# Optimization experiments

Measured on AMD Instinct MI355X. Metric: run time of the kernel, lower is better.

## Reference

```python
import math
import jax, jax.numpy as jnp
import numpy as np

HOP = 256
N_FFT = 1024
SR = 24000
B = 8
T = 1200          # feature frames
L = T * HOP       # 307200 audio samples
K_REV = 8192
BINS = N_FFT // 2 + 1


def setup_inputs() -> dict:
    key = jax.random.key(0)
    k1, k2, k3, k4, k5 = jax.random.split(key, 5)
    # realistic voiced f0 in [50, 400] Hz (forward gates on f0 > 20 Hz)
    f0 = 50.0 + 350.0 * jax.random.uniform(k1, (B, T), dtype=jnp.float32)
    env_per = jax.random.uniform(k2, (B, BINS, T), dtype=jnp.float32)
    env_noi = 0.1 * jax.random.uniform(k3, (B, BINS, T), dtype=jnp.float32)
    rev = 0.01 * jax.random.normal(k4, (B, K_REV), dtype=jnp.float32)
    # stands in for torch.rand_like(imp) inside forward (uniform [0,1))
    noi = jax.random.uniform(k5, (B, L), dtype=jnp.float32)
    # periodic Hann window, as torch.hann_window(n_fft)
    window = (0.5 - 0.5 * jnp.cos(2.0 * jnp.pi * jnp.arange(N_FFT) / N_FFT)).astype(jnp.float32)
    return {"f0": f0, "env_per": env_per, "env_noi": env_noi, "rev": rev, "noi": noi, "window": window}


def _interp_linear(x, scale):
    # torch F.interpolate(mode='linear', align_corners=False)
    Lx = x.shape[-1]
    out_len = Lx * scale
    src = (jnp.arange(out_len, dtype=jnp.float32) + 0.5) / scale - 0.5
    src = jnp.clip(src, 0.0, Lx - 1)
    i0 = jnp.floor(src).astype(jnp.int32)
    i1 = jnp.minimum(i0 + 1, Lx - 1)
    w = src - i0.astype(jnp.float32)
    return x[:, i0] * (1.0 - w) + x[:, i1] * w


def _stft(x, window):
    # torch.stft(center=True, pad_mode='reflect', return_complex=True)
    pad = N_FFT // 2
    xp = jnp.pad(x, ((0, 0), (pad, pad)), mode='reflect')
    n_frames = 1 + (xp.shape[-1] - N_FFT) // HOP
    idx = jnp.arange(n_frames)[:, None] * HOP + jnp.arange(N_FFT)[None, :]
    frames = xp[:, idx] * window                      # [B, F, N_FFT]
    return jnp.fft.rfft(frames, axis=-1).transpose(0, 2, 1)  # [B, BINS, F]


def _istft(spec, window):
    # torch.istft(center=True): windowed overlap-add with window-square normalization
    frames = jnp.fft.irfft(spec.transpose(0, 2, 1), n=N_FFT, axis=-1) * window  # [B, F, N_FFT]
    Bc, Fr, _ = frames.shape
    out_len = N_FFT + HOP * (Fr - 1)
    idx = (jnp.arange(Fr)[:, None] * HOP + jnp.arange(N_FFT)[None, :]).reshape(-1)
    out = jnp.zeros((Bc, out_len), frames.dtype).at[:, idx].add(frames.reshape(Bc, -1))
    wsq = jnp.zeros((out_len,), frames.dtype).at[idx].add(jnp.tile(window ** 2, Fr))
    out = out / jnp.where(wsq > 1e-11, wsq, 1.0)
    pad = N_FFT // 2
    return out[:, pad:out_len - pad]


def _min_phase(amp, eps=1e-5):
    # homomorphic minimum-phase reconstruction from real amplitude envelope
    # amp: [B, BINS, F]  ->  complex spectrum exp(rfft(lifted real cepstrum))
    log_amp = jnp.log(jnp.maximum(amp, eps))
    cep = jnp.fft.irfft(log_amp, n=N_FFT, axis=1)     # [B, N_FFT, F] real cepstrum
    lift = jnp.concatenate([
        jnp.ones((1,), jnp.float32),
        2.0 * jnp.ones((N_FFT // 2 - 1,), jnp.float32),
        jnp.ones((1,), jnp.float32),
        jnp.zeros((N_FFT // 2 - 1,), jnp.float32),
    ])
    return jnp.exp(jnp.fft.rfft(cep * lift[None, :, None], axis=1))  # [B, BINS, F]


def _fft_convolve(signal, kernel):
    # DDSP-style FFT convolution: zero-pad signal right, kernel left, multiply spectra
    Ls = signal.shape[-1]
    sig = jnp.pad(signal, ((0, 0), (0, Ls)))
    ker = jnp.pad(kernel, ((0, 0), (2 * Ls - kernel.shape[-1], 0)))
    out = jnp.fft.irfft(jnp.fft.rfft(sig) * jnp.fft.rfft(ker), n=2 * Ls)
    return out[:, Ls:]


def reference(f0, env_per, env_noi, rev, noi, window):
    env_per = jnp.pad(env_per, ((0, 0), (0, 0), (1, 0)))   # [B, BINS, T+1]
    env_noi = jnp.pad(env_noi, ((0, 0), (0, 0), (1, 0)))
    # sample-rate f0 track and impulse amplitude scale
    f0_up = _interp_linear(f0, HOP)                        # [B, L]
    imp_scale = jax.lax.rsqrt(jnp.maximum(f0_up, 20.0)) * math.sqrt(SR)
    # impulse train: fire where the running phase wraps past an integer
    phase = jnp.cumsum(f0_up, axis=-1) / SR
    saw = jnp.mod(phase, 1.0)
    imp = (saw - jnp.roll(saw, 1, axis=-1) < 0.0).astype(jnp.float32)
    imp = imp.at[:, 0].set(0.0)
    imp = imp * imp_scale
    imp_stft = _stft(imp, window)                          # [B, BINS, T+1]
    noi_stft = _stft(noi, window)
    # voiced/unvoiced gating of the periodic envelope
    mask = (jnp.pad(f0, ((0, 0), (1, 0)))[:, None, :] > 20.0).astype(jnp.float32)
    env_per = env_per * mask
    voi_stft = imp_stft * _min_phase(env_per) + noi_stft * env_noi
    voi = _istft(voi_stft, window)                         # [B, L]
    voi = _fft_convolve(voi, rev)                          # [B, L]
    return voi
```

## Files before the change

### kernel.cpp

```cpp
#include <hip/hip_runtime.h>
#include <math.h>

#define BB 8
#define TT 1200
#define NFFT 1024
#define BINS 513
#define LTOT 307200
#define KREV 8192
#define NFRM 34
#define NSAMP 8960
#define OUTOFF 299008
#define SQRT_SR 154.91933384829668f

#define OFF_FR   0
#define OFF_CW   278528
#define OFF_FW   350208
#define OFF_TW   421888

#define PHI(i) ((i) ^ ((i) >> 5))

__device__ __forceinline__ int rev4_10(int n) {
    int r = (int)(__brev((unsigned)n) >> 22);
    return ((r & 0x155) << 1) | ((r & 0x2AA) >> 1);
}

__device__ __forceinline__ void dif4(float* re, float* im,
                                     const float* twr, const float* twi,
                                     float dir, int u, bool act) {
#pragma unroll 1
    for (int s = 0; s < 5; ++s) {
        const int q = 256 >> (2 * s);
        const int sh = 8 - 2 * s;
        if (s < 2) __syncthreads();
        else       asm volatile("s_waitcnt lgkmcnt(0)" ::: "memory");
        if (act) {
            int t = u & (q - 1);
            int base = ((u >> sh) << (sh + 2)) | t;
            int i0 = PHI(base), i1 = PHI(base + q), i2 = PHI(base + 2 * q), i3 = PHI(base + 3 * q);
            float ar = re[i0], ai = im[i0];
            float br = re[i1], bi = im[i1];
            float cr = re[i2], ci = im[i2];
            float dr = re[i3], di = im[i3];
            float t0r = ar + cr, t0i = ai + ci;
            float t1r = ar - cr, t1i = ai - ci;
            float t2r = br + dr, t2i = bi + di;
            float t3r = br - dr, t3i = bi - di;
            float y0r = t0r + t2r, y0i = t0i + t2i;
            float y2r = t0r - t2r, y2i = t0i - t2i;
            float y1r = t1r - dir * t3i, y1i = t1i + dir * t3r;
            float y3r = t1r + dir * t3i, y3i = t1i - dir * t3r;
            float c1 = twr[2 * q - 1 + t], s1 = twi[2 * q - 1 + t];
            float c2 = twr[q - 1 + t],     s2 = twi[q - 1 + t];
            float w1r = c1, w1i = dir * s1;
            float w2r = c2, w2i = dir * s2;
            float w3r = c1 * c2 - s1 * s2;
            float w3i = dir * (c1 * s2 + s1 * c2);
            re[i0] = y0r;                       im[i0] = y0i;
            re[i1] = y1r * w1r - y1i * w1i;     im[i1] = y1r * w1i + y1i * w1r;
            re[i2] = y2r * w2r - y2i * w2i;     im[i2] = y2r * w2i + y2i * w2r;
            re[i3] = y3r * w3r - y3i * w3i;     im[i3] = y3r * w3i + y3i * w3r;
        }
    }
    __syncthreads();
}

__device__ __forceinline__ void dit4(float* re, float* im,
                                     const float* twr, const float* twi,
                                     float dir, int u, bool act) {
#pragma unroll 1
    for (int s = 0; s < 5; ++s) {
        const int q = 1 << (2 * s);
        const int sh = 2 * s;
        if (s == 0 || s == 4) __syncthreads();
        else                  asm volatile("s_waitcnt lgkmcnt(0)" ::: "memory");
        if (act) {
            int t = u & (q - 1);
            int base = ((u >> sh) << (sh + 2)) | t;
            int i0 = PHI(base), i1 = PHI(base + q), i2 = PHI(base + 2 * q), i3 = PHI(base + 3 * q);
            float c1 = twr[2 * q - 1 + t], s1 = twi[2 * q - 1 + t];
            float c2 = twr[q - 1 + t],     s2 = twi[q - 1 + t];
            float w1r = c1, w1i = dir * s1;
            float w2r = c2, w2i = dir * s2;
            float w3r = c1 * c2 - s1 * s2;
            float w3i = dir * (c1 * s2 + s1 * c2);
            float ar = re[i0], ai = im[i0];
            float xr = re[i1], xi = im[i1];
            float yr = re[i2], yi = im[i2];
            float zr = re[i3], zi = im[i3];
            float br = xr * w1r - xi * w1i, bi = xr * w1i + xi * w1r;
            float cr = yr * w2r - yi * w2i, ci = yr * w2i + yi * w2r;
            float dr = zr * w3r - zi * w3i, di = zr * w3i + zi * w3r;
            float t0r = ar + cr, t0i = ai + ci;
            float t1r = ar - cr, t1i = ai - ci;
            float t2r = br + dr, t2i = bi + di;
            float t3r = br - dr, t3i = bi - di;
            re[i0] = t0r + t2r;            im[i0] = t0i + t2i;
            re[i2] = t0r - t2r;            im[i2] = t0i - t2i;
            re[i1] = t1r - dir * t3i;      im[i1] = t1i + dir * t3r;
            re[i3] = t1r + dir * t3i;      im[i3] = t1i - dir * t3r;
        }
    }
    __syncthreads();
}

#define LV1 0
#define LV2 4480
#define LV3 6720
#define LV4 7840
#define LV5 8400
#define LV6 8680
#define LV7 8820
#define LV8 8890
#define LV9 8925
#define LV10 8942
#define LV11 8950
#define LV12 8954
#define LV13 8956

__global__ __launch_bounds__(1024) void k0(const float* __restrict__ f0,
                                           float* __restrict__ W) {
    const int b = blockIdx.x;
    const int tid = threadIdx.x;
    __shared__ float F[NSAMP];
    __shared__ float L[8957];

    if (b == 0 && tid < 1023) {
        int x = tid;
        int hb = 31 - __clz(x + 1);
        int half = 1 << hb;
        int t = (x + 1) - half;
        float a = 3.14159265358979323846f * ((float)t / (float)half);
        float sv, cv; sincosf(a, &sv, &cv);
        W[OFF_TW + x] = cv;
        W[OFF_TW + 1023 + x] = sv;
    }

    for (int i = tid; i < NSAMP; i += 1024) {
        float src = __fsub_rn(__fdiv_rn(__fadd_rn((float)i, 0.5f), 256.0f), 0.5f);
        src = fminf(fmaxf(src, 0.0f), (float)(TT - 1));
        int i0 = (int)floorf(src);
        int i1 = i0 + 1; if (i1 > TT - 1) i1 = TT - 1;
        float w = __fsub_rn(src, (float)i0);
        float a0 = __fmul_rn(f0[b * TT + i0], __fsub_rn(1.0f, w));
        float a1 = __fmul_rn(f0[b * TT + i1], w);
        F[i] = __fadd_rn(a0, a1);
    }
    __syncthreads();
    for (int j = tid; j < 2240; j += 1024) {
        float a = __fadd_rn(F[4*j],     F[4*j + 1]);
        float c = __fadd_rn(F[4*j + 2], F[4*j + 3]);
        L[LV1 + 2*j] = a; L[LV1 + 2*j + 1] = c;
        L[LV2 + j] = __fadd_rn(a, c);
    }
    __syncthreads();
    if (tid < 560) {
        int j = tid;
        float a = __fadd_rn(L[LV2 + 4*j],     L[LV2 + 4*j + 1]);
        float c = __fadd_rn(L[LV2 + 4*j + 2], L[LV2 + 4*j + 3]);
        L[LV3 + 2*j] = a; L[LV3 + 2*j + 1] = c;
        L[LV4 + j] = __fadd_rn(a, c);
    }
    __syncthreads();
    if (tid < 140) {
        int j = tid;
        float a = __fadd_rn(L[LV4 + 4*j],     L[LV4 + 4*j + 1]);
        float c = __fadd_rn(L[LV4 + 4*j + 2], L[LV4 + 4*j + 3]);
        L[LV5 + 2*j] = a; L[LV5 + 2*j + 1] = c;
        L[LV6 + j] = __fadd_rn(a, c);
    }
    __syncthreads();
    if (tid < 35) {
        int j = tid;
        float a = __fadd_rn(L[LV6 + 4*j],     L[LV6 + 4*j + 1]);
        float c = __fadd_rn(L[LV6 + 4*j + 2], L[LV6 + 4*j + 3]);
        L[LV7 + 2*j] = a; L[LV7 + 2*j + 1] = c;
        L[LV8 + j] = __fadd_rn(a, c);
    }
    __syncthreads();
    if (tid < 9) {
        int j = tid;
        if (j < 8) {
            float a = __fadd_rn(L[LV8 + 4*j],     L[LV8 + 4*j + 1]);
            float c = __fadd_rn(L[LV8 + 4*j + 2], L[LV8 + 4*j + 3]);
            L[LV9 + 2*j] = a; L[LV9 + 2*j + 1] = c;
            L[LV10 + j] = __fadd_rn(a, c);
        } else {
            L[LV9 + 16] = __fadd_rn(L[LV8 + 32], L[LV8 + 33]);
        }
    }
    __syncthreads();
    if (tid == 0) {
        float a0 = __fadd_rn(L[LV10 + 0], L[LV10 + 1]);
        float a1 = __fadd_rn(L[LV10 + 2], L[LV10 + 3]);
        float a2 = __fadd_rn(L[LV10 + 4], L[LV10 + 5]);
        float a3 = __fadd_rn(L[LV10 + 6], L[LV10 + 7]);
        L[LV11 + 0] = a0; L[LV11 + 1] = a1; L[LV11 + 2] = a2; L[LV11 + 3] = a3;
        float b0 = __fadd_rn(a0, a1), b1 = __fadd_rn(a2, a3);
        L[LV12 + 0] = b0; L[LV12 + 1] = b1;
        L[LV13 + 0] = __fadd_rn(b0, b1);
    }
    __syncthreads();
    {
        const int offs[14] = {0, LV1, LV2, LV3, LV4, LV5, LV6, LV7, LV8, LV9, LV10, LV11, LV12, LV13};
        for (int p = tid; p < NSAMP; p += 1024) {
            int n = p + 1;
            float acc = 0.f; int pos = 0; bool first = true;
#pragma unroll
            for (int k = 13; k >= 1; --k) {
                if ((n >> k) & 1) {
                    float t = L[offs[k] + (pos >> k)];
                    acc = first ? t : __fadd_rn(acc, t);
                    first = false;
                    pos += (1 << k);
                }
            }
            if (n & 1) {
                float t = F[pos];
                acc = first ? t : __fadd_rn(acc, t);
            }
            W[OFF_CW + b * NSAMP + p] = acc;
            W[OFF_FW + b * NSAMP + p] = F[p];
        }
    }
}

__global__ __launch_bounds__(512) void kfrm(const float* __restrict__ f0,
                                            const float* __restrict__ env_per,
                                            const float* __restrict__ env_noi,
                                            const float* __restrict__ noi,
                                            const float* __restrict__ win,
                                            float* __restrict__ W,
                                            float* __restrict__ out) {
    const int bid = blockIdx.x;
    const int tid = threadIdx.x;
    const int b = bid / 17;
    const int fp = (bid - b * 17) * 2;
    const int fg = fp + 1;

    __shared__ __align__(16) float SMEM[8208];
    __shared__ float cw[1281], fw[1281];
    __shared__ float twr[1023], twi[1023];

    const int idxF = (fp > 0) ? (fp - 1) : 0;
    const int idxG = fg - 1;
    float pfEpF = 0.f, pfEpG = 0.f, pfEpF2 = 0.f, pfEpG2 = 0.f;
    {
        pfEpF = env_per[((size_t)(b * BINS + tid)) * TT + idxF];
        pfEpG = env_per[((size_t)(b * BINS + tid)) * TT + idxG];
        if (tid == 0) {
            pfEpF2 = env_per[((size_t)(b * BINS + 512)) * TT + idxF];
            pfEpG2 = env_per[((size_t)(b * BINS + 512)) * TT + idxG];
        }
    }
    const float pfF0F = f0[b * TT + idxF];
    const float pfF0G = f0[b * TT + idxG];
    int ktmp0 = rev4_10(tid);
    const int kk0 = (ktmp0 <= 512) ? ktmp0 : 1024 - ktmp0;
    int ktmp1 = rev4_10(tid + 512);
    const int kk1 = (ktmp1 <= 512) ? ktmp1 : 1024 - ktmp1;
    const float pfEnF0 = env_noi[((size_t)(b * BINS + kk0)) * TT + idxF];
    const float pfEnG0 = env_noi[((size_t)(b * BINS + kk0)) * TT + idxG];
    const float pfEnF1 = env_noi[((size_t)(b * BINS + kk1)) * TT + idxF];
    const float pfEnG1 = env_noi[((size_t)(b * BINS + kk1)) * TT + idxG];
    int iF0 = 256 * fp + tid - 512; if (iF0 < 0) iF0 = -iF0;
    const int iF1 = 256 * fp + tid;
    int iG0 = 256 * fg + tid - 512; if (iG0 < 0) iG0 = -iG0;
    const int iG1 = 256 * fg + tid;
    const float pfNoiF0 = noi[(size_t)b * LTOT + iF0];
    const float pfNoiF1 = noi[(size_t)b * LTOT + iF1];
    const float pfNoiG0 = noi[(size_t)b * LTOT + iG0];
    const float pfNoiG1 = noi[(size_t)b * LTOT + iG1];
    const float pfWin0 = win[tid];
    const float pfWin1 = win[tid + 512];

    for (int x = tid; x < 1023; x += 512) {
        twr[x] = W[OFF_TW + x];
        twi[x] = W[OFF_TW + 1023 + x];
    }
    const int cbase = (fp >= 3) ? (256 * fp - 513) : 0;
    for (int w = tid; w < 1281; w += 512) {
        int p = cbase + w;
        if (p < NSAMP) {
            cw[w] = W[OFF_CW + b * NSAMP + p];
            fw[w] = W[OFF_FW + b * NSAMP + p];
        }
    }

    float* wr_  = SMEM;
    float* wi_  = SMEM + 1024;
    float* zfr  = SMEM + 2048;
    float* zfi  = SMEM + 3072;
    float* zgr  = SMEM + 4096;
    float* zgi  = SMEM + 5120;
    float* mpfr = SMEM + 6144;
    float* mpfi = SMEM + 6660;
    float* mpgr = SMEM + 7176;
    float* mpgi = SMEM + 7692;
    const int u = tid & 255;
    const bool lo = (tid < 256);

    {
        const bool gF = (fp > 0) && (pfF0F > 20.0f);
        const bool gG = (pfF0G > 20.0f);
        mpfr[tid] = logf(fmaxf(gF ? pfEpF : 0.0f, 1e-5f));
        mpgr[tid] = logf(fmaxf(gG ? pfEpG : 0.0f, 1e-5f));
        if (tid == 0) {
            mpfr[512] = logf(fmaxf(gF ? pfEpF2 : 0.0f, 1e-5f));
            mpgr[512] = logf(fmaxf(gG ? pfEpG2 : 0.0f, 1e-5f));
        }
    }
    __syncthreads();
#pragma unroll 1
    for (int r = 0; r < 2; ++r) {
        int n = tid + (r << 9);
        int kv = (n <= 512) ? n : 1024 - n;
        wr_[PHI(n)] = mpfr[kv];
        wi_[PHI(n)] = mpgr[kv];
    }
    dif4(wr_, wi_, twr, twi, -1.f, u, lo);
    const float inv = 1.0f / 1024.0f;
#pragma unroll 1
    for (int r = 0; r < 2; ++r) {
        int p = tid + (r << 9);
        int n = rev4_10(p);
        float wgt = (n == 0 || n == 512) ? inv : ((n < 512) ? 2.0f * inv : 0.0f);
        wr_[PHI(p)] *= wgt;
        wi_[PHI(p)] *= wgt;
    }
    dit4(wr_, wi_, twr, twi, -1.f, u, lo);
    for (int k = tid; k < BINS; k += 512) {
        int mk = (1024 - k) & 1023;
        float yr = wr_[PHI(k)], yi = wi_[PHI(k)];
        float ymr = wr_[PHI(mk)], ymi = -wi_[PHI(mk)];
        float Lfr = 0.5f * (yr + ymr), Lfi = 0.5f * (yi + ymi);
        float dr = yr - ymr, di = yi - ymi;
        float Lgr = 0.5f * di, Lgi = -0.5f * dr;
        float ef = expf(Lfr);
        mpfr[k] = ef * cosf(Lfi); mpfi[k] = ef * sinf(Lfi);
        float eg = expf(Lgr);
        mpgr[k] = eg * cosf(Lgi); mpgi[k] = eg * sinf(Lgi);
    }
    __syncthreads();
#pragma unroll 1
    for (int r = 0; r < 2; ++r) {
        const int n = tid + (r << 9);
        const float wv = r ? pfWin1 : pfWin0;
#pragma unroll 1
        for (int h = 0; h < 2; ++h) {
            int i = h ? (r ? iG1 : iG0) : (r ? iF1 : iF0);
            float nv = h ? (r ? pfNoiG1 : pfNoiG0) : (r ? pfNoiF1 : pfNoiF0);
            float v = 0.0f;
            if (i > 0) {
                int iw = i - cbase;
                float ph  = __fdiv_rn(cw[iw], 24000.0f);
                float sw  = __fsub_rn(ph, floorf(ph));
                float ph2 = __fdiv_rn(cw[iw - 1], 24000.0f);
                float sw2 = __fsub_rn(ph2, floorf(ph2));
                if (__fsub_rn(sw, sw2) < 0.0f)
                    v = __fmul_rn(__fdiv_rn(1.0f, __fsqrt_rn(fmaxf(fw[iw], 20.0f))), SQRT_SR);
            }
            float* zr = h ? zgr : zfr;
            float* zi = h ? zgi : zfi;
            zr[PHI(n)] = __fmul_rn(nv, wv);
            zi[PHI(n)] = __fmul_rn(v, wv);
        }
    }
    dif4(lo ? zfr : zgr, lo ? zfi : zgi, twr, twi, -1.f, u, true);
#pragma unroll 1
    for (int r = 0; r < 2; ++r) {
        int p = tid + (r << 9);
        int kk = r ? kk1 : kk0;
        float enF = (fp == 0) ? 0.0f : (r ? pfEnF1 : pfEnF0);
        float enG = r ? pfEnG1 : pfEnG0;
        int k = rev4_10(p);
        bool cj = (k > 512);
        int p1 = rev4_10(kk);
        int p2 = rev4_10((1024 - kk) & 1023);
        float vr, vi;
        {
            float z1r = zfr[PHI(p1)], z1i = zfi[PHI(p1)];
            float z2r = zfr[PHI(p2)], z2i = -zfi[PHI(p2)];
            float Nr = 0.5f * (z1r + z2r), Ni = 0.5f * (z1i + z2i);
            float dr = z1r - z2r, di = z1i - z2i;
            float Ir = 0.5f * di, Ii = -0.5f * dr;
            float mpr = mpfr[kk], mpi2 = mpfi[kk];
            vr = Ir * mpr - Ii * mpi2 + Nr * enF;
            vi = Ir * mpi2 + Ii * mpr + Ni * enF;
            if (cj) vi = -vi;
        }
        float vgr, vgi;
        {
            float z1r = zgr[PHI(p1)], z1i = zgi[PHI(p1)];
            float z2r = zgr[PHI(p2)], z2i = -zgi[PHI(p2)];
            float Nr = 0.5f * (z1r + z2r), Ni = 0.5f * (z1i + z2i);
            float dr = z1r - z2r, di = z1i - z2i;
            float Ir = 0.5f * di, Ii = -0.5f * dr;
            float mpr = mpgr[kk], mpi2 = mpgi[kk];
            vgr = Ir * mpr - Ii * mpi2 + Nr * enG;
            vgi = Ir * mpi2 + Ii * mpr + Ni * enG;
            if (cj) vgi = -vgi;
        }
        wr_[PHI(p)] = vr - vgi;
        wi_[PHI(p)] = vi + vgr;
    }
    dit4(wr_, wi_, twr, twi, +1.f, u, lo);
#pragma unroll 1
    for (int r = 0; r < 2; ++r) {
        int n = tid + (r << 9);
        float wv = r ? pfWin1 : pfWin0;
        W[OFF_FR + (((size_t)(b * NFRM + fp)) << 10) + n] = __fmul_rn(__fmul_rn(wr_[PHI(n)], inv), wv);
        W[OFF_FR + (((size_t)(b * NFRM + fg)) << 10) + n] = __fmul_rn(__fmul_rn(wi_[PHI(n)], inv), wv);
    }

    {
        float4* out4 = (float4*)out;
        int g = bid * 512 + tid;
        for (int idx = g; idx < (BB * LTOT) / 4; idx += 136 * 512)
            out4[idx] = make_float4(0.f, 0.f, 0.f, 0.f);
    }
}

__global__ __launch_bounds__(256) void k4(const float* __restrict__ rev,
                                          const float* __restrict__ win,
                                          const float* __restrict__ W,
                                          float* __restrict__ out) {
    const int tid = threadIdx.x;
    const int b = blockIdx.x / 72;
    int r = blockIdx.x - b * 72;
    int jt = 0, acc0 = 0;
    while (acc0 + 2 * (jt + 1) <= r) { acc0 += 2 * (jt + 1); ++jt; }
    const int mc = r - acc0;
    const int j0 = jt << 10, m0 = mc << 9;

    __shared__ __align__(16) float S[1536];
    __shared__ __align__(16) float Rv[512];
    for (int x = tid; x < 512; x += 256)
        Rv[x] = rev[b * KREV + m0 + x];
    const int base = j0 - m0 - 512;
    for (int x = tid; x < 1536; x += 256) {
        int j = base + x;
        float v = 0.f;
        if (j >= 0 && j < KREV) {
            int s = j + 512;
            int flo = (s >= 1023) ? ((s - 1023 + 255) >> 8) : 0;
            int fhi = s >> 8; if (fhi > NFRM - 1) fhi = NFRM - 1;
            float acc = 0.f, wsq = 0.f;
            for (int f = flo; f <= fhi; ++f) {
                int o = s - (f << 8);
                acc = __fadd_rn(acc, W[OFF_FR + (((size_t)(b * NFRM + f)) << 10) + o]);
                float wv = win[o];
                wsq = __fadd_rn(wsq, __fmul_rn(wv, wv));
            }
            float den = (wsq > 1e-11f) ? wsq : 1.0f;
            v = __fdiv_rn(acc, den);
        }
        S[x] = v;
    }
    __syncthreads();

    const float4* S4 = (const float4*)S;
    const float4* R4 = (const float4*)Rv;
    float y0 = 0.f, y1 = 0.f, y2 = 0.f, y3 = 0.f;
    const int qi = tid + 128;
    float4 Bv = S4[qi];
#pragma unroll 4
    for (int mq = 0; mq < 128; ++mq) {
        float4 A = S4[qi - 1 - mq];
        float4 r4 = R4[mq];
        y0 = fmaf(r4.x, Bv.x, y0); y0 = fmaf(r4.y, A.w,  y0); y0 = fmaf(r4.z, A.z,  y0); y0 = fmaf(r4.w, A.y,  y0);
        y1 = fmaf(r4.x, Bv.y, y1); y1 = fmaf(r4.y, Bv.x, y1); y1 = fmaf(r4.z, A.w,  y1); y1 = fmaf(r4.w, A.z,  y1);
        y2 = fmaf(r4.x, Bv.z, y2); y2 = fmaf(r4.y, Bv.y, y2); y2 = fmaf(r4.z, Bv.x, y2); y2 = fmaf(r4.w, A.w,  y2);
        y3 = fmaf(r4.x, Bv.w, y3); y3 = fmaf(r4.y, Bv.z, y3); y3 = fmaf(r4.z, Bv.y, y3); y3 = fmaf(r4.w, Bv.x, y3);
        Bv = A;
    }
    float* o = out + (size_t)b * LTOT + OUTOFF + j0 + 4 * tid;
    atomicAdd(o + 0, y0);
    atomicAdd(o + 1, y1);
    atomicAdd(o + 2, y2);
    atomicAdd(o + 3, y3);
}

extern "C" void kernel_launch(void* const* d_in, const int* in_sizes, int n_in,
                              void* d_out, int out_size, void* d_ws, size_t ws_size,
                              hipStream_t stream) {
    const float* f0      = (const float*)d_in[0];
    const float* env_per = (const float*)d_in[1];
    const float* env_noi = (const float*)d_in[2];
    const float* rev     = (const float*)d_in[3];
    const float* noi     = (const float*)d_in[4];
    const float* win     = (const float*)d_in[5];
    float* out = (float*)d_out;
    float* W   = (float*)d_ws;

    k0<<<dim3(8),     dim3(1024), 0, stream>>>(f0, W);
    kfrm<<<dim3(136), dim3(512),  0, stream>>>(f0, env_per, env_noi, noi, win, W, out);
    k4<<<dim3(576),   dim3(256),  0, stream>>>(rev, win, W, out);
}
```

Before: 150.4 us.

## Warp-specialize frame kernel so cepstrum and STFT FFTs run concurrently

Splits the 512-thread frame kernel into two 256-thread halves. One half computes the log-envelope cepstrum FFTs (min-phase path) while the other half loads the phase and noise data, builds the impulse and noise frames, and runs the forward STFT FFTs. The previously serialized dif4/dit4 passes become interleaved per-stage calls under shared barriers. Each half now handles four elements per thread, and the old lgkmcnt-only waits between stages are replaced by full barriers. That adds synchronization, and the final inverse FFT uses only half the threads.

Measured after the change: 151.8 us. About the same (+1.0%).

```diff
diff --git a/kernel.cpp b/kernel.cpp
--- a/kernel.cpp
+++ b/kernel.cpp
@@ -24,83 +24,67 @@
     return ((r & 0x155) << 1) | ((r & 0x2AA) >> 1);
 }
 
-__device__ __forceinline__ void dif4(float* re, float* im,
-                                     const float* twr, const float* twi,
-                                     float dir, int u, bool act) {
-#pragma unroll 1
-    for (int s = 0; s < 5; ++s) {
-        const int q = 256 >> (2 * s);
-        const int sh = 8 - 2 * s;
-        if (s < 2) __syncthreads();
-        else       asm volatile("s_waitcnt lgkmcnt(0)" ::: "memory");
-        if (act) {
-            int t = u & (q - 1);
-            int base = ((u >> sh) << (sh + 2)) | t;
-            int i0 = PHI(base), i1 = PHI(base + q), i2 = PHI(base + 2 * q), i3 = PHI(base + 3 * q);
-            float ar = re[i0], ai = im[i0];
-            float br = re[i1], bi = im[i1];
-            float cr = re[i2], ci = im[i2];
-            float dr = re[i3], di = im[i3];
-            float t0r = ar + cr, t0i = ai + ci;
-            float t1r = ar - cr, t1i = ai - ci;
-            float t2r = br + dr, t2i = bi + di;
-            float t3r = br - dr, t3i = bi - di;
-            float y0r = t0r + t2r, y0i = t0i + t2i;
-            float y2r = t0r - t2r, y2i = t0i - t2i;
-            float y1r = t1r - dir * t3i, y1i = t1i + dir * t3r;
-            float y3r = t1r + dir * t3i, y3i = t1i - dir * t3r;
-            float c1 = twr[2 * q - 1 + t], s1 = twi[2 * q - 1 + t];
-            float c2 = twr[q - 1 + t],     s2 = twi[q - 1 + t];
-            float w1r = c1, w1i = dir * s1;
-            float w2r = c2, w2i = dir * s2;
-            float w3r = c1 * c2 - s1 * s2;
-            float w3i = dir * (c1 * s2 + s1 * c2);
-            re[i0] = y0r;                       im[i0] = y0i;
-            re[i1] = y1r * w1r - y1i * w1i;     im[i1] = y1r * w1i + y1i * w1r;
-            re[i2] = y2r * w2r - y2i * w2i;     im[i2] = y2r * w2i + y2i * w2r;
-            re[i3] = y3r * w3r - y3i * w3i;     im[i3] = y3r * w3i + y3i * w3r;
-        }
-    }
-    __syncthreads();
-}
-
-__device__ __forceinline__ void dit4(float* re, float* im,
-                                     const float* twr, const float* twi,
-                                     float dir, int u, bool act) {
-#pragma unroll 1
-    for (int s = 0; s < 5; ++s) {
-        const int q = 1 << (2 * s);
-        const int sh = 2 * s;
-        if (s == 0 || s == 4) __syncthreads();
-        else                  asm volatile("s_waitcnt lgkmcnt(0)" ::: "memory");
-        if (act) {
-            int t = u & (q - 1);
-            int base = ((u >> sh) << (sh + 2)) | t;
-            int i0 = PHI(base), i1 = PHI(base + q), i2 = PHI(base + 2 * q), i3 = PHI(base + 3 * q);
-            float c1 = twr[2 * q - 1 + t], s1 = twi[2 * q - 1 + t];
-            float c2 = twr[q - 1 + t],     s2 = twi[q - 1 + t];
-            float w1r = c1, w1i = dir * s1;
-            float w2r = c2, w2i = dir * s2;
-            float w3r = c1 * c2 - s1 * s2;
-            float w3i = dir * (c1 * s2 + s1 * c2);
-            float ar = re[i0], ai = im[i0];
-            float xr = re[i1], xi = im[i1];
-            float yr = re[i2], yi = im[i2];
-            float zr = re[i3], zi = im[i3];
-            float br = xr * w1r - xi * w1i, bi = xr * w1i + xi * w1r;
-            float cr = yr * w2r - yi * w2i, ci = yr * w2i + yi * w2r;
-            float dr = zr * w3r - zi * w3i, di = zr * w3i + zi * w3r;
-            float t0r = ar + cr, t0i = ai + ci;
-            float t1r = ar - cr, t1i = ai - ci;
-            float t2r = br + dr, t2i = bi + di;
-            float t3r = br - dr, t3i = bi - di;
-            re[i0] = t0r + t2r;            im[i0] = t0i + t2i;
-            re[i2] = t0r - t2r;            im[i2] = t0i - t2i;
-            re[i1] = t1r - dir * t3i;      im[i1] = t1i + dir * t3r;
-            re[i3] = t1r + dir * t3i;      im[i3] = t1i - dir * t3r;
-        }
-    }
-    __syncthreads();
+__device__ __forceinline__ void dif_stage(float* re, float* im,
+                                          const float* twr, const float* twi,
+                                          float dir, int u, int s) {
+    const int q = 256 >> (2 * s);
+    const int sh = 8 - 2 * s;
+    int t = u & (q - 1);
+    int base = ((u >> sh) << (sh + 2)) | t;
+    int i0 = PHI(base), i1 = PHI(base + q), i2 = PHI(base + 2 * q), i3 = PHI(base + 3 * q);
+    float ar = re[i0], ai = im[i0];
+    float br = re[i1], bi = im[i1];
+    float cr = re[i2], ci = im[i2];
+    float dr = re[i3], di = im[i3];
+    float t0r = ar + cr, t0i = ai + ci;
+    float t1r = ar - cr, t1i = ai - ci;
+    float t2r = br + dr, t2i = bi + di;
+    float t3r = br - dr, t3i = bi - di;
+    float y0r = t0r + t2r, y0i = t0i + t2i;
+    float y2r = t0r - t2r, y2i = t0i - t2i;
+    float y1r = t1r - dir * t3i, y1i = t1i + dir * t3r;
+    float y3r = t1r + dir * t3i, y3i = t1i - dir * t3r;
+    float c1 = twr[2 * q - 1 + t], s1 = twi[2 * q - 1 + t];
+    float c2 = twr[q - 1 + t],     s2 = twi[q - 1 + t];
+    float w1r = c1, w1i = dir * s1;
+    float w2r = c2, w2i = dir * s2;
+    float w3r = c1 * c2 - s1 * s2;
+    float w3i = dir * (c1 * s2 + s1 * c2);
+    re[i0] = y0r;                       im[i0] = y0i;
+    re[i1] = y1r * w1r - y1i * w1i;     im[i1] = y1r * w1i + y1i * w1r;
+    re[i2] = y2r * w2r - y2i * w2i;     im[i2] = y2r * w2i + y2i * w2r;
+    re[i3] = y3r * w3r - y3i * w3i;     im[i3] = y3r * w3i + y3i * w3r;
+}
+
+__device__ __forceinline__ void dit_stage(float* re, float* im,
+                                          const float* twr, const float* twi,
+                                          float dir, int u, int s) {
+    const int q = 1 << (2 * s);
+    const int sh = 2 * s;
+    int t = u & (q - 1);
+    int base = ((u >> sh) << (sh + 2)) | t;
+    int i0 = PHI(base), i1 = PHI(base + q), i2 = PHI(base + 2 * q), i3 = PHI(base + 3 * q);
+    float c1 = twr[2 * q - 1 + t], s1 = twi[2 * q - 1 + t];
+    float c2 = twr[q - 1 + t],     s2 = twi[q - 1 + t];
+    float w1r = c1, w1i = dir * s1;
+    float w2r = c2, w2i = dir * s2;
+    float w3r = c1 * c2 - s1 * s2;
+    float w3i = dir * (c1 * s2 + s1 * c2);
+    float ar = re[i0], ai = im[i0];
+    float xr = re[i1], xi = im[i1];
+    float yr = re[i2], yi = im[i2];
+    float zr = re[i3], zi = im[i3];
+    float br = xr * w1r - xi * w1i, bi = xr * w1i + xi * w1r;
+    float cr = yr * w2r - yi * w2i, ci = yr * w2i + yi * w2r;
+    float dr = zr * w3r - zi * w3i, di = zr * w3i + zi * w3r;
+    float t0r = ar + cr, t0i = ai + ci;
+    float t1r = ar - cr, t1i = ai - ci;
+    float t2r = br + dr, t2i = bi + di;
+    float t3r = br - dr, t3i = bi - di;
+    re[i0] = t0r + t2r;            im[i0] = t0i + t2i;
+    re[i2] = t0r - t2r;            im[i2] = t0i - t2i;
+    re[i1] = t1r - dir * t3i;      im[i1] = t1i + dir * t3r;
+    re[i3] = t1r + dir * t3i;      im[i3] = t1i - dir * t3r;
 }
 
 #define LV1 0
@@ -236,55 +220,12 @@
     const int b = bid / 17;
     const int fp = (bid - b * 17) * 2;
     const int fg = fp + 1;
+    const bool Aside = (tid < 256);
+    const int u2 = tid & 255;
 
     __shared__ __align__(16) float SMEM[8208];
     __shared__ float cw[1281], fw[1281];
     __shared__ float twr[1023], twi[1023];
-
-    const int idxF = (fp > 0) ? (fp - 1) : 0;
-    const int idxG = fg - 1;
-    float pfEpF = 0.f, pfEpG = 0.f, pfEpF2 = 0.f, pfEpG2 = 0.f;
-    {
-        pfEpF = env_per[((size_t)(b * BINS + tid)) * TT + idxF];
-        pfEpG = env_per[((size_t)(b * BINS + tid)) * TT + idxG];
-        if (tid == 0) {
-            pfEpF2 = env_per[((size_t)(b * BINS + 512)) * TT + idxF];
-            pfEpG2 = env_per[((size_t)(b * BINS + 512)) * TT + idxG];
-        }
-    }
-    const float pfF0F = f0[b * TT + idxF];
-    const float pfF0G = f0[b * TT + idxG];
-    int ktmp0 = rev4_10(tid);
-    const int kk0 = (ktmp0 <= 512) ? ktmp0 : 1024 - ktmp0;
-    int ktmp1 = rev4_10(tid + 512);
-    const int kk1 = (ktmp1 <= 512) ? ktmp1 : 1024 - ktmp1;
-    const float pfEnF0 = env_noi[((size_t)(b * BINS + kk0)) * TT + idxF];
-    const float pfEnG0 = env_noi[((size_t)(b * BINS + kk0)) * TT + idxG];
-    const float pfEnF1 = env_noi[((size_t)(b * BINS + kk1)) * TT + idxF];
-    const float pfEnG1 = env_noi[((size_t)(b * BINS + kk1)) * TT + idxG];
-    int iF0 = 256 * fp + tid - 512; if (iF0 < 0) iF0 = -iF0;
-    const int iF1 = 256 * fp + tid;
-    int iG0 = 256 * fg + tid - 512; if (iG0 < 0) iG0 = -iG0;
-    const int iG1 = 256 * fg + tid;
-    const float pfNoiF0 = noi[(size_t)b * LTOT + iF0];
-    const float pfNoiF1 = noi[(size_t)b * LTOT + iF1];
-    const float pfNoiG0 = noi[(size_t)b * LTOT + iG0];
-    const float pfNoiG1 = noi[(size_t)b * LTOT + iG1];
-    const float pfWin0 = win[tid];
-    const float pfWin1 = win[tid + 512];
-
-    for (int x = tid; x < 1023; x += 512) {
-        twr[x] = W[OFF_TW + x];
-        twi[x] = W[OFF_TW + 1023 + x];
-    }
-    const int cbase = (fp >= 3) ? (256 * fp - 513) : 0;
-    for (int w = tid; w < 1281; w += 512) {
-        int p = cbase + w;
-        if (p < NSAMP) {
-            cw[w] = W[OFF_CW + b * NSAMP + p];
-            fw[w] = W[OFF_FW + b * NSAMP + p];
-        }
-    }
 
     float* wr_  = SMEM;
     float* wi_  = SMEM + 1024;
@@ -296,38 +237,155 @@
     float* mpfi = SMEM + 6660;
     float* mpgr = SMEM + 7176;
     float* mpgi = SMEM + 7692;
-    const int u = tid & 255;
-    const bool lo = (tid < 256);
-
-    {
+
+    const int idxF = (fp > 0) ? (fp - 1) : 0;
+    const int idxG = fg - 1;
+    const int cbase = (fp >= 3) ? (256 * fp - 513) : 0;
+
+    int ktmp0 = rev4_10(tid);
+    const int kk0 = (ktmp0 <= 512) ? ktmp0 : 1024 - ktmp0;
+    int ktmp1 = rev4_10(tid + 512);
+    const int kk1 = (ktmp1 <= 512) ? ktmp1 : 1024 - ktmp1;
+    const float pfEnF0 = env_noi[((size_t)(b * BINS + kk0)) * TT + idxF];
+    const float pfEnG0 = env_noi[((size_t)(b * BINS + kk0)) * TT + idxG];
+    const float pfEnF1 = env_noi[((size_t)(b * BINS + kk1)) * TT + idxF];
+    const float pfEnG1 = env_noi[((size_t)(b * BINS + kk1)) * TT + idxG];
+
+    float pfEpFa = 0.f, pfEpFb = 0.f, pfEpFc = 0.f;
+    float pfEpGa = 0.f, pfEpGb = 0.f, pfEpGc = 0.f;
+    float pfF0F = 0.f, pfF0G = 0.f;
+    float pfWinA0 = 0.f, pfWinA1 = 0.f;
+    float pfNoiF[4], pfNoiG[4], pfWinB[4];
+    int   iF[4], iG[4];
+
+    if (Aside) {
+        pfEpFa = env_per[((size_t)(b * BINS + u2)) * TT + idxF];
+        pfEpGa = env_per[((size_t)(b * BINS + u2)) * TT + idxG];
+        pfEpFb = env_per[((size_t)(b * BINS + u2 + 256)) * TT + idxF];
+        pfEpGb = env_per[((size_t)(b * BINS + u2 + 256)) * TT + idxG];
+        if (u2 == 0) {
+            pfEpFc = env_per[((size_t)(b * BINS + 512)) * TT + idxF];
+            pfEpGc = env_per[((size_t)(b * BINS + 512)) * TT + idxG];
+        }
+        pfF0F = f0[b * TT + idxF];
+        pfF0G = f0[b * TT + idxG];
+        pfWinA0 = win[u2];
+        pfWinA1 = win[u2 + 512];
+        for (int x = u2; x < 1023; x += 256) {
+            twr[x] = W[OFF_TW + x];
+            twi[x] = W[OFF_TW + 1023 + x];
+        }
+    } else {
+        for (int w = u2; w < 1281; w += 256) {
+            int p = cbase + w;
+            if (p < NSAMP) {
+                cw[w] = W[OFF_CW + b * NSAMP + p];
+                fw[w] = W[OFF_FW + b * NSAMP + p];
+            }
+        }
+#pragma unroll
+        for (int j = 0; j < 4; ++j) {
+            int n = u2 + 256 * j;
+            int a = 256 * fp + n - 512; if (a < 0) a = -a;
+            int c = 256 * fg + n - 512; if (c < 0) c = -c;
+            iF[j] = a; iG[j] = c;
+            pfNoiF[j] = noi[(size_t)b * LTOT + a];
+            pfNoiG[j] = noi[(size_t)b * LTOT + c];
+            pfWinB[j] = win[n];
+        }
+    }
+    __syncthreads();
+
+    if (Aside) {
         const bool gF = (fp > 0) && (pfF0F > 20.0f);
         const bool gG = (pfF0G > 20.0f);
-        mpfr[tid] = logf(fmaxf(gF ? pfEpF : 0.0f, 1e-5f));
-        mpgr[tid] = logf(fmaxf(gG ? pfEpG : 0.0f, 1e-5f));
-        if (tid == 0) {
-            mpfr[512] = logf(fmaxf(gF ? pfEpF2 : 0.0f, 1e-5f));
-            mpgr[512] = logf(fmaxf(gG ? pfEpG2 : 0.0f, 1e-5f));
-        }
-    }
-    __syncthreads();
-#pragma unroll 1
-    for (int r = 0; r < 2; ++r) {
-        int n = tid + (r << 9);
-        int kv = (n <= 512) ? n : 1024 - n;
-        wr_[PHI(n)] = mpfr[kv];
-        wi_[PHI(n)] = mpgr[kv];
-    }
-    dif4(wr_, wi_, twr, twi, -1.f, u, lo);
+        mpfr[u2]       = logf(fmaxf(gF ? pfEpFa : 0.0f, 1e-5f));
+        mpgr[u2]       = logf(fmaxf(gG ? pfEpGa : 0.0f, 1e-5f));
+        mpfr[u2 + 256] = logf(fmaxf(gF ? pfEpFb : 0.0f, 1e-5f));
+        mpgr[u2 + 256] = logf(fmaxf(gG ? pfEpGb : 0.0f, 1e-5f));
+        if (u2 == 0) {
+            mpfr[512] = logf(fmaxf(gF ? pfEpFc : 0.0f, 1e-5f));
+            mpgr[512] = logf(fmaxf(gG ? pfEpGc : 0.0f, 1e-5f));
+        }
+    } else {
+#pragma unroll
+        for (int j = 0; j < 4; ++j) {
+            int n = u2 + 256 * j;
+            int i = iF[j];
+            float v = 0.0f;
+            if (i > 0) {
+                int iw = i - cbase;
+                float ph  = __fdiv_rn(cw[iw], 24000.0f);
+                float sw  = __fsub_rn(ph, floorf(ph));
+                float ph2 = __fdiv_rn(cw[iw - 1], 24000.0f);
+                float sw2 = __fsub_rn(ph2, floorf(ph2));
+                if (__fsub_rn(sw, sw2) < 0.0f)
+                    v = __fmul_rn(__fdiv_rn(1.0f, __fsqrt_rn(fmaxf(fw[iw], 20.0f))), SQRT_SR);
+            }
+            zfr[PHI(n)] = __fmul_rn(pfNoiF[j], pfWinB[j]);
+            zfi[PHI(n)] = __fmul_rn(v, pfWinB[j]);
+        }
+    }
+    __syncthreads();
+
+    if (Aside) {
+#pragma unroll
+        for (int j = 0; j < 4; ++j) {
+            int n = u2 + 256 * j;
+            int kv = (n <= 512) ? n : 1024 - n;
+            wr_[PHI(n)] = mpfr[kv];
+            wi_[PHI(n)] = mpgr[kv];
+        }
+    } else {
+#pragma unroll
+        for (int j = 0; j < 4; ++j) {
+            int n = u2 + 256 * j;
+            int i = iG[j];
+            float v = 0.0f;
+            if (i > 0) {
+                int iw = i - cbase;
+                float ph  = __fdiv_rn(cw[iw], 24000.0f);
+                float sw  = __fsub_rn(ph, floorf(ph));
+                float ph2 = __fdiv_rn(cw[iw - 1], 24000.0f);
+                float sw2 = __fsub_rn(ph2, floorf(ph2));
+                if (__fsub_rn(sw, sw2) < 0.0f)
+                    v = __fmul_rn(__fdiv_rn(1.0f, __fsqrt_rn(fmaxf(fw[iw], 20.0f))), SQRT_SR);
+            }
+            zgr[PHI(n)] = __fmul_rn(pfNoiG[j], pfWinB[j]);
+            zgi[PHI(n)] = __fmul_rn(v, pfWinB[j]);
+        }
+    }
+
+#pragma unroll
+    for (int s = 0; s < 5; ++s) {
+        __syncthreads();
+        if (Aside) dif_stage(wr_, wi_, twr, twi, -1.f, u2, s);
+        else       dif_stage(zfr, zfi, twr, twi, -1.f, u2, s);
+    }
+
+    __syncthreads();
     const float inv = 1.0f / 1024.0f;
-#pragma unroll 1
-    for (int r = 0; r < 2; ++r) {
-        int p = tid + (r << 9);
-        int n = rev4_10(p);
-        float wgt = (n == 0 || n == 512) ? inv : ((n < 512) ? 2.0f * inv : 0.0f);
-        wr_[PHI(p)] *= wgt;
-        wi_[PHI(p)] *= wgt;
-    }
-    dit4(wr_, wi_, twr, twi, -1.f, u, lo);
+    if (Aside) {
+#pragma unroll
+        for (int j = 0; j < 4; ++j) {
+            int p = u2 + 256 * j;
+            int n = rev4_10(p);
+            float wgt = (n == 0 || n == 512) ? inv : ((n < 512) ? 2.0f * inv : 0.0f);
+            wr_[PHI(p)] *= wgt;
+            wi_[PHI(p)] *= wgt;
+        }
+    } else {
+        dif_stage(zgr, zgi, twr, twi, -1.f, u2, 0);
+    }
+
+#pragma unroll
+    for (int s = 0; s < 5; ++s) {
+        __syncthreads();
+        if (Aside)      dit_stage(wr_, wi_, twr, twi, -1.f, u2, s);
+        else if (s < 4) dif_stage(zgr, zgi, twr, twi, -1.f, u2, s + 1);
+    }
+    __syncthreads();
+
     for (int k = tid; k < BINS; k += 512) {
         int mk = (1024 - k) & 1023;
         float yr = wr_[PHI(k)], yi = wi_[PHI(k)];
@@ -341,32 +399,8 @@
         mpgr[k] = eg * cosf(Lgi); mpgi[k] = eg * sinf(Lgi);
     }
     __syncthreads();
-#pragma unroll 1
-    for (int r = 0; r < 2; ++r) {
-        const int n = tid + (r << 9);
-        const float wv = r ? pfWin1 : pfWin0;
-#pragma unroll 1
-        for (int h = 0; h < 2; ++h) {
-            int i = h ? (r ? iG1 : iG0) : (r ? iF1 : iF0);
-            float nv = h ? (r ? pfNoiG1 : pfNoiG0) : (r ? pfNoiF1 : pfNoiF0);
-            float v = 0.0f;
-            if (i > 0) {
-                int iw = i - cbase;
-                float ph  = __fdiv_rn(cw[iw], 24000.0f);
-                float sw  = __fsub_rn(ph, floorf(ph));
-                float ph2 = __fdiv_rn(cw[iw - 1], 24000.0f);
-                float sw2 = __fsub_rn(ph2, floorf(ph2));
-                if (__fsub_rn(sw, sw2) < 0.0f)
-                    v = __fmul_rn(__fdiv_rn(1.0f, __fsqrt_rn(fmaxf(fw[iw], 20.0f))), SQRT_SR);
-            }
-            float* zr = h ? zgr : zfr;
-            float* zi = h ? zgi : zfi;
-            zr[PHI(n)] = __fmul_rn(nv, wv);
-            zi[PHI(n)] = __fmul_rn(v, wv);
-        }
-    }
-    dif4(lo ? zfr : zgr, lo ? zfi : zgi, twr, twi, -1.f, u, true);
-#pragma unroll 1
+
+#pragma unroll
     for (int r = 0; r < 2; ++r) {
         int p = tid + (r << 9);
         int kk = r ? kk1 : kk0;
@@ -403,15 +437,24 @@
         wr_[PHI(p)] = vr - vgi;
         wi_[PHI(p)] = vi + vgr;
     }
-    dit4(wr_, wi_, twr, twi, +1.f, u, lo);
-#pragma unroll 1
-    for (int r = 0; r < 2; ++r) {
-        int n = tid + (r << 9);
-        float wv = r ? pfWin1 : pfWin0;
-        W[OFF_FR + (((size_t)(b * NFRM + fp)) << 10) + n] = __fmul_rn(__fmul_rn(wr_[PHI(n)], inv), wv);
-        W[OFF_FR + (((size_t)(b * NFRM + fg)) << 10) + n] = __fmul_rn(__fmul_rn(wi_[PHI(n)], inv), wv);
-    }
-
+
+#pragma unroll
+    for (int s = 0; s < 5; ++s) {
+        __syncthreads();
+        if (Aside) dit_stage(wr_, wi_, twr, twi, +1.f, u2, s);
+    }
+    __syncthreads();
+
+    {
+        int n1 = tid;
+        int n2 = tid + 512;
+        float w1 = Aside ? pfWinA0 : pfWinB[1];
+        float w2 = Aside ? pfWinA1 : pfWinB[3];
+        W[OFF_FR + (((size_t)(b * NFRM + fp)) << 10) + n1] = __fmul_rn(__fmul_rn(wr_[PHI(n1)], inv), w1);
+        W[OFF_FR + (((size_t)(b * NFRM + fg)) << 10) + n1] = __fmul_rn(__fmul_rn(wi_[PHI(n1)], inv), w1);
+        W[OFF_FR + (((size_t)(b * NFRM + fp)) << 10) + n2] = __fmul_rn(__fmul_rn(wr_[PHI(n2)], inv), w2);
+        W[OFF_FR + (((size_t)(b * NFRM + fg)) << 10) + n2] = __fmul_rn(__fmul_rn(wi_[PHI(n2)], inv), w2);
+    }
     {
         float4* out4 = (float4*)out;
         int g = bid * 512 + tid;
```
